# Kernel tuning notes

Measured on AMD Instinct MI355X. Metric: run time of the kernel, lower is better.

Reference implementation:

```python
import jax, jax.numpy as jnp
import numpy as np

H = 50      # hidden_size (fixed in source)
IN = 7      # input_size = len(features)
B = 1024    # batch
T = 512     # seq_len
FC1 = 25
OUT = 1


def setup_inputs() -> dict:
    key = jax.random.key(0)
    ks = jax.random.split(key, 24)
    s = 1.0 / np.sqrt(H)  # PyTorch LSTM/Linear default uniform init scale

    def u(k, shape):
        return jax.random.uniform(k, shape, jnp.float32, -s, s)

    d = {"x": jax.random.normal(ks[0], (B, T, IN), jnp.float32)}
    # 4 stacked LSTM layers total: lstm1 has 2 layers (in=7 then 50), lstm2 has 2 layers (in=50)
    in_sizes = [IN, H, H, H]
    for l, isz in enumerate(in_sizes):
        d[f"Wih{l}"] = u(ks[1 + 4 * l], (4 * H, isz))
        d[f"Whh{l}"] = u(ks[2 + 4 * l], (4 * H, H))
        d[f"bih{l}"] = u(ks[3 + 4 * l], (4 * H,))
        d[f"bhh{l}"] = u(ks[4 + 4 * l], (4 * H,))
    d["W1"] = u(ks[17], (FC1, H))
    d["b1"] = u(ks[18], (FC1,))
    d["W2"] = u(ks[19], (OUT, FC1))
    d["b2"] = u(ks[20], (OUT,))
    return d


def _lstm_layer(x, Wih, Whh, bih, bhh):
    # x: [B, T, in] -> hidden sequence [B, T, H]. PyTorch gate order: i, f, g, o.
    b, t, _ = x.shape
    h = Whh.shape[1]
    # Precompute input projection for all timesteps in one big GEMM: [T, B, 4H]
    xp = jnp.einsum('bti,gi->tbg', x, Wih) + (bih + bhh)

    def step(carry, xt):
        hs, cs = carry
        gates = xt + hs @ Whh.T                      # [B, 4H]
        i, f, g, o = jnp.split(gates, 4, axis=-1)
        i = jax.nn.sigmoid(i)
        f = jax.nn.sigmoid(f)
        g = jnp.tanh(g)
        o = jax.nn.sigmoid(o)
        cs = f * cs + i * g
        hs = o * jnp.tanh(cs)
        return (hs, cs), hs

    h0 = jnp.zeros((b, h), x.dtype)
    _, hseq = jax.lax.scan(step, (h0, h0), xp)       # hseq: [T, B, H]
    return hseq.transpose(1, 0, 2)


def reference(x, Wih0, Whh0, bih0, bhh0, Wih1, Whh1, bih1, bhh1,
              Wih2, Whh2, bih2, bhh2, Wih3, Whh3, bih3, bhh3,
              W1, b1, W2, b2):
    out = x
    layers = [(Wih0, Whh0, bih0, bhh0), (Wih1, Whh1, bih1, bhh1),
              (Wih2, Whh2, bih2, bhh2), (Wih3, Whh3, bih3, bhh3)]
    for Wih, Whh, bih, bhh in layers:
        out = _lstm_layer(out, Wih, Whh, bih, bhh)
    h = out[:, -1, :]                                # last timestep [B, H]
    # dropout is identity in eval mode
    h = jax.nn.relu(h @ W1.T + b1)
    return h @ W2.T + b2                             # [B, 1]
```

## Files before the change

### kernel.cpp

```cpp
#include <hip/hip_runtime.h>


#define H 50
#define INSZ 7
#define TT 512
#define NL 4
#define FC1N 25
#define BPG 4
#define NBLK 256
#define NTHREADS 1024
#define HS 80
#define BIASL 56
#define XRING 64
#define XB 32

typedef _Float16 half_t;
typedef __attribute__((ext_vector_type(8))) _Float16 half8_t;
typedef __attribute__((ext_vector_type(4))) float float4_t;

struct Params {
  const float* x;
  const float* Wih[NL];
  const float* Whh[NL];
  const float* bih[NL];
  const float* bhh[NL];
  const float* W1;
  const float* b1;
  const float* W2;
  const float* b2;
  float* out;
};

__device__ __forceinline__ float sigf(float x) {
  return __builtin_amdgcn_rcpf(1.0f + __builtin_amdgcn_exp2f(-1.442695041f * x));
}
__device__ __forceinline__ float tanh_fast(float x) {
  return 2.0f * __builtin_amdgcn_rcpf(1.0f + __builtin_amdgcn_exp2f(-2.885390082f * x)) - 1.0f;
}

#define MFMA16(A, B, C) __builtin_amdgcn_mfma_f32_16x16x32_f16((A), (B), (C), 0, 0, 0)

__global__ __launch_bounds__(NTHREADS, 4) void lstm_r6(Params p) {
  __shared__ __align__(16) half_t Hbuf[NL][2][BPG][HS];
  __shared__ __align__(16) half_t Xstage[XRING][BPG][XB];
  __shared__ float fc_h[BPG][H];
  __shared__ float fc1_buf[BPG][FC1N];

  const int tid = threadIdx.x;
  const int b0 = blockIdx.x * BPG;
  const int lane = tid & 63;
  const int quad = lane >> 4;
  const int col = lane & 15;
  const int glay = tid >> 8;
  const int wl = (((tid >> 6) & 3) + glay) & 3;

  half8_t afrag[4][4];
#pragma unroll
  for (int t4 = 0; t4 < 4; ++t4) {
#pragma unroll
    for (int g = 0; g < 4; ++g) {
      half8_t v;
#pragma unroll
      for (int j = 0; j < 8; ++j) {
        const int r = wl * 64 + t4 * 16 + col;
        const int u = r >> 2, q = r & 3;
        const int k = g * 32 + quad * 8 + j;
        float wv = 0.0f;
        if (u < H) {
          const int row = q * H + u;
          if (glay == 0) {
            if (k < INSZ) wv = p.Wih[0][row * INSZ + k];
            else if (k >= 64 && (k - 64) < H) wv = p.Whh[0][row * H + (k - 64)];
            else if (k == 120) wv = p.bih[0][row] + p.bhh[0][row];
          } else {
            if (k < H) wv = p.Wih[glay][row * H + k];
            else if (k == BIASL) wv = p.bih[glay][row] + p.bhh[glay][row];
            else if (k >= 64 && (k - 64) < H) wv = p.Whh[glay][row * H + (k - 64)];
          }
        }
        v[j] = (half_t)wv;
      }
      afrag[t4][g] = v;
    }
  }

  {
    unsigned* hz = (unsigned*)Hbuf;
    const int nh = NL * 2 * BPG * HS / 2;
    for (int i = tid; i < nh; i += NTHREADS) hz[i] = 0u;
    unsigned* xz = (unsigned*)Xstage;
    const int nx = XRING * BPG * XB / 2;
    for (int i = tid; i < nx; i += NTHREADS) xz[i] = 0u;
  }
  __syncthreads();
  if (tid < 32) {
    const int l = tid >> 3, pr = (tid >> 2) & 1, b = tid & 3;
    Hbuf[l][pr][b][BIASL] = (half_t)1.0f;
  }
  for (int i = tid; i < XRING * BPG * INSZ; i += NTHREADS) {
    const int t = i / (BPG * INSZ), rem = i % (BPG * INSZ);
    const int b = rem / INSZ, k = rem % INSZ;
    Xstage[t][b][k] = (half_t)p.x[((size_t)(b0 + b) * TT + t) * INSZ + k];
  }
  __syncthreads();

  const int bb = col & 3;
  const int tsel = col >> 2;
  const int uu = 16 * wl + 4 * tsel + quad;
  const bool updact = (uu < H);

  const half_t* inb[2];
  inb[0] = (glay == 0) ? (const half_t*)Xstage : &Hbuf[glay - 1][1][bb][quad * 8];
  inb[1] = (glay == 0) ? (const half_t*)Xstage : &Hbuf[glay - 1][0][bb][quad * 8];
  const half_t* ownb[2] = {&Hbuf[glay][0][bb][quad * 8], &Hbuf[glay][1][bb][quad * 8]};
  half_t* stb[2] = {&Hbuf[glay][1][bb][uu], &Hbuf[glay][0][bb][uu]};

  const int pe = glay & 1, po = pe ^ 1;
  const half_t* in_e = inb[pe];
  const half_t* in_o = inb[po];
  const half_t* own_e = ownb[pe];
  const half_t* own_o = ownb[po];
  half_t* st_e = stb[pe];
  half_t* st_o = stb[po];
  const half_t* xrb = &Xstage[0][bb][quad * 8];

  const bool xwave = (glay == 0) && (wl == 3);
  const int rb = lane >> 5;
  const int rt = lane & 31;

  float cst = 0.0f;

#define TICK_BODY(PIN, POWN, PST, FCW)                                          \
  {                                                                             \
    const float4_t fz_ = {0.0f, 0.0f, 0.0f, 0.0f};                              \
    float4_t a0 = fz_, a1 = fz_, a2 = fz_, a3 = fz_;                            \
    if (glay == 0) {                                                            \
      const half8_t v0 = *(const half8_t*)(PIN);                                \
      const half8_t v2 = *(const half8_t*)(POWN);                               \
      const half8_t v3 = *(const half8_t*)((POWN) + 32);                        \
      if (wl != 3) {                                                            \
        a0 = MFMA16(afrag[0][0], v0, a0); a1 = MFMA16(afrag[1][0], v0, a1);     \
        a2 = MFMA16(afrag[2][0], v0, a2); a3 = MFMA16(afrag[3][0], v0, a3);     \
        a0 = MFMA16(afrag[0][2], v2, a0); a1 = MFMA16(afrag[1][2], v2, a1);     \
        a2 = MFMA16(afrag[2][2], v2, a2); a3 = MFMA16(afrag[3][2], v2, a3);     \
        a0 = MFMA16(afrag[0][3], v3, a0); a1 = MFMA16(afrag[1][3], v3, a1);     \
        a2 = MFMA16(afrag[2][3], v3, a2); a3 = MFMA16(afrag[3][3], v3, a3);     \
      } else {                                                                  \
        a0 = MFMA16(afrag[0][0], v0, a0);                                       \
        a0 = MFMA16(afrag[0][2], v2, a0);                                       \
        a0 = MFMA16(afrag[0][3], v3, a0);                                       \
      }                                                                         \
    } else {                                                                    \
      const half8_t v0 = *(const half8_t*)(PIN);                                \
      const half8_t v1 = *(const half8_t*)((PIN) + 32);                         \
      const half8_t v2 = *(const half8_t*)(POWN);                               \
      const half8_t v3 = *(const half8_t*)((POWN) + 32);                        \
      if (wl != 3) {                                                            \
        a0 = MFMA16(afrag[0][0], v0, a0); a1 = MFMA16(afrag[1][0], v0, a1);     \
        a2 = MFMA16(afrag[2][0], v0, a2); a3 = MFMA16(afrag[3][0], v0, a3);     \
        a0 = MFMA16(afrag[0][1], v1, a0); a1 = MFMA16(afrag[1][1], v1, a1);     \
        a2 = MFMA16(afrag[2][1], v1, a2); a3 = MFMA16(afrag[3][1], v1, a3);     \
        a0 = MFMA16(afrag[0][2], v2, a0); a1 = MFMA16(afrag[1][2], v2, a1);     \
        a2 = MFMA16(afrag[2][2], v2, a2); a3 = MFMA16(afrag[3][2], v2, a3);     \
        a0 = MFMA16(afrag[0][3], v3, a0); a1 = MFMA16(afrag[1][3], v3, a1);     \
        a2 = MFMA16(afrag[2][3], v3, a2); a3 = MFMA16(afrag[3][3], v3, a3);     \
      } else {                                                                  \
        a0 = MFMA16(afrag[0][0], v0, a0);                                       \
        a0 = MFMA16(afrag[0][1], v1, a0);                                       \
        a0 = MFMA16(afrag[0][2], v2, a0);                                       \
        a0 = MFMA16(afrag[0][3], v3, a0);                                       \
      }                                                                         \
    }                                                                           \
    if (updact) {                                                               \
      const float4_t g01 = (col & 4) ? a1 : a0;                                 \
      const float4_t g23 = (col & 4) ? a3 : a2;                                 \
      const float4_t ga = (col & 8) ? g23 : g01;                                \
      const float gi = sigf(ga[0]);                                             \
      const float gf = sigf(ga[1]);                                             \
      const float gg = tanh_fast(ga[2]);                                        \
      const float go = sigf(ga[3]);                                             \
      cst = gf * cst + gi * gg;                                                 \
      const float h = go * tanh_fast(cst);                                      \
      *(PST) = (half_t)h;                                                       \
      if (FCW) fc_h[bb][uu] = h;                                                \
    }                                                                           \
  }

  for (int s = 0; s < 3; ++s) {
    const int t = s - glay;
    if (t >= 0) {
      const int par = t & 1;
      const half_t* pin = (glay == 0) ? (xrb + (t & 63) * (BPG * XB)) : inb[par];
      TICK_BODY(pin, ownb[par], stb[par], false)
    }
    __syncthreads();
  }

  for (int s = 3; s < 511; s += 2) {
    {
      const int t = s - glay;
      const half_t* pin = (glay == 0) ? (xrb + (s & 63) * (BPG * XB)) : in_o;
      TICK_BODY(pin, own_o, st_o, false)
    }
    __syncthreads();
    {
      const int s2 = s + 1;
      if (xwave && (s2 & 31) == 8 && s2 < 480) {
        const int tb = (s2 & ~31) + 32;
#pragma unroll
        for (int pp = 0; pp < 2; ++pp) {
          const int b = rb + 2 * pp;
          const int t = tb + rt;
          const float* src = &p.x[((size_t)(b0 + b) * TT + t) * INSZ];
          half_t* dst = &Xstage[t & 63][b][0];
#pragma unroll
          for (int k = 0; k < INSZ; ++k) dst[k] = (half_t)src[k];
        }
      }
      const int t = s2 - glay;
      const half_t* pin = (glay == 0) ? (xrb + (s2 & 63) * (BPG * XB)) : in_e;
      TICK_BODY(pin, own_e, st_e, false)
    }
    __syncthreads();
  }

  for (int s = 511; s < TT + NL - 1; ++s) {
    const int t = s - glay;
    if (t < TT) {
      const int par = t & 1;
      const half_t* pin = (glay == 0) ? (xrb + (t & 63) * (BPG * XB)) : inb[par];
      const bool fcw = (glay == NL - 1) && (t == TT - 1);
      TICK_BODY(pin, ownb[par], stb[par], fcw)
    }
    __syncthreads();
  }

  if (tid < BPG * FC1N) {
    const int b = tid / FC1N, j = tid % FC1N;
    const float* w = p.W1 + j * H;
    float a = p.b1[j];
#pragma unroll
    for (int k = 0; k < H; ++k) a += fc_h[b][k] * w[k];
    fc1_buf[b][j] = fmaxf(a, 0.0f);
  }
  __syncthreads();
  if (tid < BPG) {
    float a = p.b2[0];
#pragma unroll
    for (int j = 0; j < FC1N; ++j) a += fc1_buf[tid][j] * p.W2[j];
    p.out[b0 + tid] = a;
  }
}

extern "C" void kernel_launch(void* const* d_in, const int* in_sizes, int n_in,
                              void* d_out, int out_size, void* d_ws, size_t ws_size,
                              hipStream_t stream) {
  Params p;
  p.x = (const float*)d_in[0];
  for (int l = 0; l < NL; ++l) {
    p.Wih[l] = (const float*)d_in[1 + 4 * l];
    p.Whh[l] = (const float*)d_in[2 + 4 * l];
    p.bih[l] = (const float*)d_in[3 + 4 * l];
    p.bhh[l] = (const float*)d_in[4 + 4 * l];
  }
  p.W1 = (const float*)d_in[17];
  p.b1 = (const float*)d_in[18];
  p.W2 = (const float*)d_in[19];
  p.b2 = (const float*)d_in[20];
  p.out = (float*)d_out;

  hipLaunchKernelGGL(lstm_r6, dim3(NBLK), dim3(NTHREADS), 0, stream, p);
}
```

Before: 489.7 us.

## Pack layer-0 input and hidden state into one ring row, share reciprocals in gates

```diff
diff --git a/kernel.cpp b/kernel.cpp
--- a/kernel.cpp
+++ b/kernel.cpp
@@ -10,9 +10,8 @@
 #define NBLK 256
 #define NTHREADS 1024
 #define HS 80
+#define RROW (BPG * HS)
 #define BIASL 56
-#define XRING 64
-#define XB 32
 
 typedef _Float16 half_t;
 typedef __attribute__((ext_vector_type(8))) _Float16 half8_t;
@@ -31,18 +30,13 @@
   float* out;
 };
 
-__device__ __forceinline__ float sigf(float x) {
-  return __builtin_amdgcn_rcpf(1.0f + __builtin_amdgcn_exp2f(-1.442695041f * x));
-}
-__device__ __forceinline__ float tanh_fast(float x) {
-  return 2.0f * __builtin_amdgcn_rcpf(1.0f + __builtin_amdgcn_exp2f(-2.885390082f * x)) - 1.0f;
-}
-
 #define MFMA16(A, B, C) __builtin_amdgcn_mfma_f32_16x16x32_f16((A), (B), (C), 0, 0, 0)
-
-__global__ __launch_bounds__(NTHREADS, 4) void lstm_r6(Params p) {
-  __shared__ __align__(16) half_t Hbuf[NL][2][BPG][HS];
-  __shared__ __align__(16) half_t Xstage[XRING][BPG][XB];
+#define EXP2F(x) __builtin_amdgcn_exp2f(x)
+#define RCPF(x) __builtin_amdgcn_rcpf(x)
+
+__global__ __launch_bounds__(NTHREADS, 4) void lstm_r7(Params p) {
+  __shared__ __align__(16) half_t Xring[64][BPG][HS];
+  __shared__ __align__(16) half_t Hbuf[NL - 1][2][BPG][HS];
   __shared__ float fc_h[BPG][H];
   __shared__ float fc1_buf[BPG][FC1N];
 
@@ -70,12 +64,16 @@
           const int row = q * H + u;
           if (glay == 0) {
             if (k < INSZ) wv = p.Wih[0][row * INSZ + k];
-            else if (k >= 64 && (k - 64) < H) wv = p.Whh[0][row * H + (k - 64)];
-            else if (k == 120) wv = p.bih[0][row] + p.bhh[0][row];
+            else if (k == 7) wv = p.bih[0][row] + p.bhh[0][row];
+            else if (k >= 8 && k < 8 + H) wv = p.Whh[0][row * H + (k - 8)];
+          } else if (glay == 1) {
+            if (k == 7) wv = p.bih[1][row] + p.bhh[1][row];
+            else if (k >= 8 && k < 8 + H) wv = p.Wih[1][row * H + (k - 8)];
+            else if (k >= 64 && k < 64 + H) wv = p.Whh[1][row * H + (k - 64)];
           } else {
             if (k < H) wv = p.Wih[glay][row * H + k];
             else if (k == BIASL) wv = p.bih[glay][row] + p.bhh[glay][row];
-            else if (k >= 64 && (k - 64) < H) wv = p.Whh[glay][row * H + (k - 64)];
+            else if (k >= 64 && k < 64 + H) wv = p.Whh[glay][row * H + (k - 64)];
           }
         }
         v[j] = (half_t)wv;
@@ -85,22 +83,24 @@
   }
 
   {
+    unsigned* xz = (unsigned*)Xring;
+    const int nx = 64 * BPG * HS / 2;
+    for (int i = tid; i < nx; i += NTHREADS) xz[i] = 0u;
     unsigned* hz = (unsigned*)Hbuf;
-    const int nh = NL * 2 * BPG * HS / 2;
+    const int nh = (NL - 1) * 2 * BPG * HS / 2;
     for (int i = tid; i < nh; i += NTHREADS) hz[i] = 0u;
-    unsigned* xz = (unsigned*)Xstage;
-    const int nx = XRING * BPG * XB / 2;
-    for (int i = tid; i < nx; i += NTHREADS) xz[i] = 0u;
   }
   __syncthreads();
-  if (tid < 32) {
+  for (int i = tid; i < 64 * BPG; i += NTHREADS)
+    Xring[i >> 2][i & 3][7] = (half_t)1.0f;
+  if (tid < (NL - 1) * 2 * BPG) {
     const int l = tid >> 3, pr = (tid >> 2) & 1, b = tid & 3;
     Hbuf[l][pr][b][BIASL] = (half_t)1.0f;
   }
-  for (int i = tid; i < XRING * BPG * INSZ; i += NTHREADS) {
+  for (int i = tid; i < 64 * BPG * INSZ; i += NTHREADS) {
     const int t = i / (BPG * INSZ), rem = i % (BPG * INSZ);
     const int b = rem / INSZ, k = rem % INSZ;
-    Xstage[t][b][k] = (half_t)p.x[((size_t)(b0 + b) * TT + t) * INSZ + k];
+    Xring[t][b][k] = (half_t)p.x[((size_t)(b0 + b) * TT + t) * INSZ + k];
   }
   __syncthreads();
 
@@ -109,12 +109,22 @@
   const int uu = 16 * wl + 4 * tsel + quad;
   const bool updact = (uu < H);
 
-  const half_t* inb[2];
-  inb[0] = (glay == 0) ? (const half_t*)Xstage : &Hbuf[glay - 1][1][bb][quad * 8];
-  inb[1] = (glay == 0) ? (const half_t*)Xstage : &Hbuf[glay - 1][0][bb][quad * 8];
-  const half_t* ownb[2] = {&Hbuf[glay][0][bb][quad * 8], &Hbuf[glay][1][bb][quad * 8]};
-  half_t* stb[2] = {&Hbuf[glay][1][bb][uu], &Hbuf[glay][0][bb][uu]};
-
+  const half_t* ring_rd0 = &Xring[0][bb][quad * 8];
+  half_t* ring_st0 = &Xring[0][bb][8 + uu];
+
+  const half_t* inb[2] = {nullptr, nullptr};
+  const half_t* ownb[2] = {nullptr, nullptr};
+  half_t* stb[2] = {nullptr, nullptr};
+  if (glay >= 1) {
+    ownb[0] = &Hbuf[glay - 1][0][bb][quad * 8];
+    ownb[1] = &Hbuf[glay - 1][1][bb][quad * 8];
+    stb[0] = &Hbuf[glay - 1][1][bb][uu];
+    stb[1] = &Hbuf[glay - 1][0][bb][uu];
+  }
+  if (glay >= 2) {
+    inb[0] = &Hbuf[glay - 2][1][bb][quad * 8];
+    inb[1] = &Hbuf[glay - 2][0][bb][quad * 8];
+  }
   const int pe = glay & 1, po = pe ^ 1;
   const half_t* in_e = inb[pe];
   const half_t* in_o = inb[po];
@@ -122,33 +132,28 @@
   const half_t* own_o = ownb[po];
   half_t* st_e = stb[pe];
   half_t* st_o = stb[po];
-  const half_t* xrb = &Xstage[0][bb][quad * 8];
 
   const bool xwave = (glay == 0) && (wl == 3);
   const int rb = lane >> 5;
   const int rt = lane & 31;
 
   float cst = 0.0f;
+  const float4_t fzc = {0.0f, 0.0f, 0.0f, 0.0f};
 
 #define TICK_BODY(PIN, POWN, PST, FCW)                                          \
   {                                                                             \
-    const float4_t fz_ = {0.0f, 0.0f, 0.0f, 0.0f};                              \
-    float4_t a0 = fz_, a1 = fz_, a2 = fz_, a3 = fz_;                            \
+    float4_t a0 = fzc, a1 = fzc, a2 = fzc, a3 = fzc;                            \
     if (glay == 0) {                                                            \
       const half8_t v0 = *(const half8_t*)(PIN);                                \
-      const half8_t v2 = *(const half8_t*)(POWN);                               \
-      const half8_t v3 = *(const half8_t*)((POWN) + 32);                        \
+      const half8_t v1 = *(const half8_t*)((PIN) + 32);                         \
       if (wl != 3) {                                                            \
         a0 = MFMA16(afrag[0][0], v0, a0); a1 = MFMA16(afrag[1][0], v0, a1);     \
         a2 = MFMA16(afrag[2][0], v0, a2); a3 = MFMA16(afrag[3][0], v0, a3);     \
-        a0 = MFMA16(afrag[0][2], v2, a0); a1 = MFMA16(afrag[1][2], v2, a1);     \
-        a2 = MFMA16(afrag[2][2], v2, a2); a3 = MFMA16(afrag[3][2], v2, a3);     \
-        a0 = MFMA16(afrag[0][3], v3, a0); a1 = MFMA16(afrag[1][3], v3, a1);     \
-        a2 = MFMA16(afrag[2][3], v3, a2); a3 = MFMA16(afrag[3][3], v3, a3);     \
+        a0 = MFMA16(afrag[0][1], v1, a0); a1 = MFMA16(afrag[1][1], v1, a1);     \
+        a2 = MFMA16(afrag[2][1], v1, a2); a3 = MFMA16(afrag[3][1], v1, a3);     \
       } else {                                                                  \
         a0 = MFMA16(afrag[0][0], v0, a0);                                       \
-        a0 = MFMA16(afrag[0][2], v2, a0);                                       \
-        a0 = MFMA16(afrag[0][3], v3, a0);                                       \
+        a0 = MFMA16(afrag[0][1], v1, a0);                                       \
       }                                                                         \
     } else {                                                                    \
       const half8_t v0 = *(const half8_t*)(PIN);                                \
@@ -175,12 +180,19 @@
       const float4_t g01 = (col & 4) ? a1 : a0;                                 \
       const float4_t g23 = (col & 4) ? a3 : a2;                                 \
       const float4_t ga = (col & 8) ? g23 : g01;                                \
-      const float gi = sigf(ga[0]);                                             \
-      const float gf = sigf(ga[1]);                                             \
-      const float gg = tanh_fast(ga[2]);                                        \
-      const float go = sigf(ga[3]);                                             \
+      const float di = 1.0f + EXP2F(-1.442695041f * ga[0]);                     \
+      const float df = 1.0f + EXP2F(-1.442695041f * ga[1]);                     \
+      const float dg = 1.0f + EXP2F(-2.885390082f * ga[2]);                     \
+      const float dq = 1.0f + EXP2F(-1.442695041f * ga[3]);                     \
+      const float r1 = RCPF(di * df);                                           \
+      const float r2 = RCPF(dg * dq);                                           \
+      const float gi = r1 * df;                                                 \
+      const float gf = r1 * di;                                                 \
+      const float gg = 2.0f * (r2 * dq) - 1.0f;                                 \
+      const float go = r2 * dg;                                                 \
       cst = gf * cst + gi * gg;                                                 \
-      const float h = go * tanh_fast(cst);                                      \
+      const float dc = 1.0f + EXP2F(-2.885390082f * cst);                       \
+      const float h = go * (2.0f * RCPF(dc) - 1.0f);                            \
       *(PST) = (half_t)h;                                                       \
       if (FCW) fc_h[bb][uu] = h;                                                \
     }                                                                           \
@@ -189,18 +201,25 @@
   for (int s = 0; s < 3; ++s) {
     const int t = s - glay;
     if (t >= 0) {
+      const half_t* rd = ring_rd0 + (s & 63) * RROW;
+      half_t* rst = ring_st0 + ((s + 1) & 63) * RROW;
       const int par = t & 1;
-      const half_t* pin = (glay == 0) ? (xrb + (t & 63) * (BPG * XB)) : inb[par];
-      TICK_BODY(pin, ownb[par], stb[par], false)
+      const half_t* pin = (glay <= 1) ? rd : inb[par];
+      const half_t* pown = (glay >= 1) ? ownb[par] : rd;
+      half_t* pst = (glay == 0) ? rst : stb[par];
+      TICK_BODY(pin, pown, pst, false)
     }
     __syncthreads();
   }
 
   for (int s = 3; s < 511; s += 2) {
     {
-      const int t = s - glay;
-      const half_t* pin = (glay == 0) ? (xrb + (s & 63) * (BPG * XB)) : in_o;
-      TICK_BODY(pin, own_o, st_o, false)
+      const half_t* rd = ring_rd0 + (s & 63) * RROW;
+      half_t* rst = ring_st0 + ((s + 1) & 63) * RROW;
+      const half_t* pin = (glay <= 1) ? rd : in_o;
+      const half_t* pown = (glay >= 1) ? own_o : rd;
+      half_t* pst = (glay == 0) ? rst : st_o;
+      TICK_BODY(pin, pown, pst, false)
     }
     __syncthreads();
     {
@@ -212,14 +231,17 @@
           const int b = rb + 2 * pp;
           const int t = tb + rt;
           const float* src = &p.x[((size_t)(b0 + b) * TT + t) * INSZ];
-          half_t* dst = &Xstage[t & 63][b][0];
+          half_t* dst = &Xring[t & 63][b][0];
 #pragma unroll
           for (int k = 0; k < INSZ; ++k) dst[k] = (half_t)src[k];
         }
       }
-      const int t = s2 - glay;
-      const half_t* pin = (glay == 0) ? (xrb + (s2 & 63) * (BPG * XB)) : in_e;
-      TICK_BODY(pin, own_e, st_e, false)
+      const half_t* rd = ring_rd0 + (s2 & 63) * RROW;
+      half_t* rst = ring_st0 + ((s2 + 1) & 63) * RROW;
+      const half_t* pin = (glay <= 1) ? rd : in_e;
+      const half_t* pown = (glay >= 1) ? own_e : rd;
+      half_t* pst = (glay == 0) ? rst : st_e;
+      TICK_BODY(pin, pown, pst, false)
     }
     __syncthreads();
   }
@@ -227,10 +249,14 @@
   for (int s = 511; s < TT + NL - 1; ++s) {
     const int t = s - glay;
     if (t < TT) {
+      const half_t* rd = ring_rd0 + (s & 63) * RROW;
+      half_t* rst = ring_st0 + ((s + 1) & 63) * RROW;
       const int par = t & 1;
-      const half_t* pin = (glay == 0) ? (xrb + (t & 63) * (BPG * XB)) : inb[par];
+      const half_t* pin = (glay <= 1) ? rd : inb[par];
+      const half_t* pown = (glay >= 1) ? ownb[par] : rd;
+      half_t* pst = (glay == 0) ? rst : stb[par];
       const bool fcw = (glay == NL - 1) && (t == TT - 1);
-      TICK_BODY(pin, ownb[par], stb[par], fcw)
+      TICK_BODY(pin, pown, pst, fcw)
     }
     __syncthreads();
   }
@@ -269,5 +295,5 @@
   p.b2 = (const float*)d_in[20];
   p.out = (float*)d_out;
 
-  hipLaunchKernelGGL(lstm_r6, dim3(NBLK), dim3(NTHREADS), 0, stream, p);
+  hipLaunchKernelGGL(lstm_r7, dim3(NBLK), dim3(NTHREADS), 0, stream, p);
 }
```

Result: slower. 510.3 us (+4.2%).
